# Optimization experiments

Hardware: AMD Instinct MI355X
Metric: run time of the kernel (lower is better)

The kernel has to match this reference:

```python
import jax, jax.numpy as jnp
import numpy as np

T, B = 128, 64
STATE_DIM, LATENT_DIM, AC_DIM, MS_DIM = 32, 16, 8, 8
STATE_EMBED, AC_EMBED, HIDDEN, OUT_DIM = 64, 16, 64, 18


def setup_inputs() -> dict:
    key = jax.random.key(0)
    ks = jax.random.split(key, 18)
    f = lambda i, shape: jax.random.normal(ks[i], shape, jnp.float32)
    s = 0.05  # param scale
    return dict(
        state=f(0, (T, B, STATE_DIM)),
        latent_mean=f(1, (T, B, LATENT_DIM)),
        latent_logvar=f(2, (T, B, LATENT_DIM)) * 0.1,
        latent_mean_t=f(3, (T, B, LATENT_DIM)),
        latent_logvar_t=f(4, (T, B, LATENT_DIM)) * 0.1,
        agent_character=f(5, (T, B, AC_DIM)),
        mental_state=f(6, (T, B, MS_DIM)),
        partner_actions=jax.random.randint(ks[7], (T, B), 0, OUT_DIM, jnp.int32),
        dones=(jax.random.uniform(ks[8], (T, B)) < 0.05).astype(jnp.float32),
        W_state=f(9, (STATE_DIM, STATE_EMBED)) * s, b_state=jnp.zeros(STATE_EMBED),
        W_ac=f(10, (AC_DIM, AC_EMBED)) * s, b_ac=jnp.zeros(AC_EMBED),
        W_embed=f(11, (STATE_EMBED + AC_EMBED, HIDDEN)) * s, b_embed=jnp.zeros(HIDDEN),
        W_hid=f(12, (AC_EMBED + MS_DIM, HIDDEN)) * s, b_hid=jnp.zeros(HIDDEN),
        Wi=f(13, (HIDDEN, 3 * HIDDEN)) * s, bi=jnp.zeros(3 * HIDDEN),
        Wh_rz=f(14, (HIDDEN, 2 * HIDDEN)) * s,
        Wh_n=f(15, (HIDDEN, HIDDEN)) * s, bh_n=jnp.zeros(HIDDEN),
        W_out=f(16, (HIDDEN, OUT_DIM)) * s, b_out=jnp.zeros(OUT_DIM),
    )


def reference(state, latent_mean, latent_logvar, latent_mean_t, latent_logvar_t,
              agent_character, mental_state, partner_actions, dones,
              W_state, b_state, W_ac, b_ac, W_embed, b_embed, W_hid, b_hid,
              Wi, bi, Wh_rz, Wh_n, bh_n, W_out, b_out):
    Tn = state.shape[0]
    # ---- KL between consecutive latent Gaussians (with N(0,I) prior at t=0) ----
    lm = jnp.concatenate((latent_mean, latent_mean_t), -1)      # (T,B,2L)
    lv = jnp.concatenate((latent_logvar, latent_logvar_t), -1)
    G = lm.shape[-1]
    am = jnp.concatenate((jnp.zeros((1,) + lm.shape[1:], lm.dtype), lm))
    al = jnp.concatenate((jnp.zeros((1,) + lv.shape[1:], lv.dtype), lv))
    mu, m = am[1:], am[:-1]
    logE, logS = al[1:], al[:-1]
    kl = 0.5 * (logS.sum(-1) - logE.sum(-1) - G
                + jnp.exp(logE - logS).sum(-1)
                + ((m - mu) ** 2 / jnp.exp(logS)).sum(-1))      # (T,B)
    kl_loss = kl.sum()
    # ---- feature extractors ----
    se = jax.nn.relu(state @ W_state + b_state)                 # (T,B,SE)
    ae = jax.nn.relu(agent_character @ W_ac + b_ac)             # (T,B,AE)
    embed = jnp.concatenate((se, ae), -1) @ W_embed + b_embed   # (T,B,H)
    hidden = jnp.concatenate((ae, mental_state), -1) @ W_hid + b_hid  # (T,B,H)
    # ---- k-batch: K=T shifted trajectories, zero-padded at the tail ----
    idx = jnp.arange(Tn)[:, None] + jnp.arange(Tn)[None, :]     # (K,T)
    valid = idx < Tn                                            # (K,T) bool
    cidx = jnp.minimum(idx, Tn - 1)
    vf = valid.astype(embed.dtype)[..., None]                   # (K,T,1)
    k_embed = embed[cidx] * vf[..., None]                       # (K,T,B,H)
    k_hidden = hidden[cidx] * vf[..., None]                     # (K,T,B,H)
    k_dones = dones[cidx] * vf                                  # (K,T,B)
    k_actions = jnp.where(valid[..., None], partner_actions[cidx], 0)  # (K,T,B)
    # fill_to_first_true: 1 up to and including the first done of each k-traj
    episode_mask = (jnp.cumsum(k_dones, axis=1) - k_dones == 0).astype(embed.dtype)  # (K,T,B)
    # ---- GRU scan over timestep axis, vectorized over (K,B) ----
    h0 = k_hidden[:, 0]                                         # (K,B,H)
    xs = (jnp.moveaxis(k_embed, 1, 0), jnp.moveaxis(k_hidden, 1, 0), jnp.moveaxis(k_dones, 1, 0))

    def step(h, x):
        x_t, h0_t, d_t = x                                      # (K,B,H),(K,B,H),(K,B)
        h = jnp.where(d_t[..., None] > 0, h0_t, h)              # reset on done
        ir, iz, i_n = jnp.split(x_t @ Wi + bi, 3, -1)
        hr, hz = jnp.split(h @ Wh_rz, 2, -1)
        r = jax.nn.sigmoid(ir + hr)
        z = jax.nn.sigmoid(iz + hz)
        n = jnp.tanh(i_n + r * (h @ Wh_n + bh_n))
        h_new = (1.0 - z) * n + z * h
        return h_new, h_new

    _, hs = jax.lax.scan(step, h0, xs)                          # (T,K,B,H)
    logp = jax.nn.log_softmax(hs @ W_out + b_out, -1)           # (T,K,B,O)
    k_act_t = jnp.moveaxis(k_actions, 1, 0)                     # (T,K,B)
    nll = -jnp.take_along_axis(logp, k_act_t[..., None], -1)[..., 0]  # (T,K,B)
    mask = valid.T[:, :, None].astype(nll.dtype) * jnp.moveaxis(episode_mask, 1, 0)
    recon_loss = (nll * mask).sum(axis=1)                       # sum over K -> (T,B)
    return kl_loss, recon_loss
```

## Files before the change

kernel.cpp:

```cpp
#include <hip/hip_runtime.h>


#define XI_OFF   0
#define HID_OFF  3145728
#define CTR_OFF  4194304

typedef float f32x16 __attribute__((ext_vector_type(16)));
typedef _Float16 h2 __attribute__((ext_vector_type(2)));

#if __has_builtin(__builtin_amdgcn_fdot2)
#define DOT2(a, b, c) __builtin_amdgcn_fdot2((a), (b), (c), false)
#else
#define DOT2(a, b, c) ((c) + (float)(a).x * (float)(b).x + (float)(a).y * (float)(b).y)
#endif

__device__ __forceinline__ h2 pack_pair(float h) {
  int hb = __builtin_bit_cast(int, h);
  int hp = __builtin_amdgcn_mov_dpp(hb, 0xB1, 0xF, 0xF, true);
  return __builtin_bit_cast(h2, __builtin_amdgcn_cvt_pkrtz(h, __builtin_bit_cast(float, hp)));
}

__global__ __launch_bounds__(256, 1) void precompute_kernel(
    const float* __restrict__ state, const float* __restrict__ ac, const float* __restrict__ ms,
    const float* __restrict__ Wst, const float* __restrict__ bst,
    const float* __restrict__ Wac, const float* __restrict__ bac,
    const float* __restrict__ Wem, const float* __restrict__ bem,
    const float* __restrict__ Whd, const float* __restrict__ bhd,
    const float* __restrict__ Wi,  const float* __restrict__ bi,
    const float* __restrict__ lm, const float* __restrict__ lv,
    const float* __restrict__ lmt, const float* __restrict__ lvt,
    _Float16* __restrict__ xi16, _Float16* __restrict__ hid16, float* __restrict__ out) {
  __shared__ float sWst[32 * 64];
  __shared__ float sWem[80 * 64];
  __shared__ float sWhd[24 * 64];
  __shared__ float sWac[8 * 16];
  __shared__ float sb[208];
  __shared__ float sin_[4][48];
  __shared__ float sse[4][80];
  __shared__ float semb[4][64];
  __shared__ float ps[4];
  int tid = threadIdx.x, lane = tid & 63, w = tid >> 6;

  if (blockIdx.x >= 256) {
    float total = 0.f;
    for (int it = 0; it < 16; ++it) {
      int idx = ((int)blockIdx.x - 256) * 256 + tid + it * 16384;
      int g = idx & 31;
      int pair = idx >> 5;
      const float* M = (g < 16) ? lm : lmt;
      const float* V = (g < 16) ? lv : lvt;
      int cur = pair * 16 + (g & 15);
      float mu = M[cur], lE = V[cur];
      float m = 0.f, lS = 0.f;
      if (pair >= 64) { m = M[cur - 1024]; lS = V[cur - 1024]; }
      float d = m - mu;
      total += 0.5f * (lS - lE - 1.f + __expf(lE - lS) + d * d * __expf(-lS));
    }
    #pragma unroll
    for (int off = 32; off; off >>= 1) total += __shfl_xor(total, off);
    if (lane == 0) ps[w] = total;
    __syncthreads();
    if (tid == 0) atomicAdd(out, ps[0] + ps[1] + ps[2] + ps[3]);
    return;
  }

  f32x16 wi0[4], wi1[4], wi2[4];
  #pragma unroll
  for (int k = 0; k < 64; ++k) {
    wi0[k >> 4][k & 15] = Wi[k * 192 + lane];
    wi1[k >> 4][k & 15] = Wi[k * 192 + 64 + lane];
    wi2[k >> 4][k & 15] = Wi[k * 192 + 128 + lane];
  }
  for (int i = tid; i < 32 * 64; i += 256) sWst[i] = Wst[i];
  for (int i = tid; i < 80 * 64; i += 256) sWem[i] = Wem[i];
  for (int i = tid; i < 24 * 64; i += 256) sWhd[i] = Whd[i];
  for (int i = tid; i < 8 * 16; i += 256) sWac[i] = Wac[i];
  if (tid < 64) sb[tid] = bst[tid];
  if (tid < 16) sb[64 + tid] = bac[tid];
  if (tid < 64) sb[80 + tid] = bem[tid];
  if (tid < 64) sb[144 + tid] = bhd[tid];
  float bi0 = bi[lane], bi1 = bi[64 + lane], bi2 = bi[128 + lane];
  __syncthreads();
  for (int cnt = 0; cnt < 8; ++cnt) {
    int pair = blockIdx.x * 32 + w * 8 + cnt;
    if (lane < 32)      sin_[w][lane] = state[pair * 32 + lane];
    else if (lane < 40) sin_[w][lane] = ac[pair * 8 + (lane - 32)];
    else if (lane < 48) sin_[w][lane] = ms[pair * 8 + (lane - 40)];
    __syncthreads();
    float se = sb[lane];
    #pragma unroll
    for (int k = 0; k < 32; ++k) se += sin_[w][k] * sWst[k * 64 + lane];
    se = fmaxf(se, 0.f);
    float ae = 0.f;
    if (lane < 16) {
      ae = sb[64 + lane];
      #pragma unroll
      for (int k = 0; k < 8; ++k) ae += sin_[w][32 + k] * sWac[k * 16 + lane];
      ae = fmaxf(ae, 0.f);
    }
    __syncthreads();
    sse[w][lane] = se;
    if (lane < 16) sse[w][64 + lane] = ae;
    __syncthreads();
    float em = sb[80 + lane];
    #pragma unroll
    for (int k = 0; k < 80; ++k) em += sse[w][k] * sWem[k * 64 + lane];
    float hd = sb[144 + lane];
    #pragma unroll
    for (int k = 0; k < 16; ++k) hd += sse[w][64 + k] * sWhd[k * 64 + lane];
    #pragma unroll
    for (int k = 0; k < 8; ++k) hd += sin_[w][40 + k] * sWhd[(16 + k) * 64 + lane];
    hid16[pair * 64 + lane] = (_Float16)hd;
    semb[w][lane] = em;
    __syncthreads();
    float x0 = bi0, x1 = bi1, x2 = bi2;
    #pragma unroll
    for (int k = 0; k < 64; ++k) {
      float e = semb[w][k];
      x0 += e * wi0[k >> 4][k & 15];
      x1 += e * wi1[k >> 4][k & 15];
      x2 += e * wi2[k >> 4][k & 15];
    }
    _Float16* xo = xi16 + pair * 192;
    xo[lane] = (_Float16)x0; xo[64 + lane] = (_Float16)x1; xo[128 + lane] = (_Float16)x2;
    __syncthreads();
  }
}

__global__ __launch_bounds__(64, 2) void rollout_kernel(
    const _Float16* __restrict__ xi16, const _Float16* __restrict__ hid16,
    const float* __restrict__ dones, const int* __restrict__ actions,
    const float* __restrict__ Whrz, const float* __restrict__ Whn,
    const float* __restrict__ bhn, const float* __restrict__ Wout,
    const float* __restrict__ bout, float* __restrict__ out,
    unsigned int* __restrict__ ctrs) {
  __shared__ __attribute__((aligned(16))) h2 sh2[32];
  __shared__ __attribute__((aligned(16))) float sloge[20];
  int lane = threadIdx.x;
  int row = (lane < 18) ? lane : 0;
  h2 Wr[32], Wz[32], Wn[32], Wo[32];
  #pragma unroll
  for (int k = 0; k < 32; ++k) {
    Wr[k] = h2{(_Float16)Whrz[(2 * k) * 128 + lane],      (_Float16)Whrz[(2 * k + 1) * 128 + lane]};
    Wz[k] = h2{(_Float16)Whrz[(2 * k) * 128 + 64 + lane], (_Float16)Whrz[(2 * k + 1) * 128 + 64 + lane]};
    Wn[k] = h2{(_Float16)Whn[(2 * k) * 64 + lane],        (_Float16)Whn[(2 * k + 1) * 64 + lane]};
    Wo[k] = h2{(_Float16)Wout[(2 * k) * 18 + row],        (_Float16)Wout[(2 * k + 1) * 18 + row]};
  }
  if (lane < 2) sloge[18 + lane] = 0.f;
  float bhn_r = bhn[lane];
  float bo_r = bout[row];
  __syncthreads();
  const uint4* shv = (const uint4*)sh2;
  int q = blockIdx.x & 7;
  while (true) {
    int i = 0;
    if (lane == 0) i = (int)atomicAdd(&ctrs[q], 1u);
    i = __shfl(i, 0);
    if (i >= 1024) break;
    int t = i >> 3, b = ((i & 7) << 3) | q;
    int u = t;
    int pr = (t << 6) | b;
    float h = (float)hid16[pr * 64 + lane];
    const _Float16* xb = xi16 + pr * 192;
    float x0 = (float)xb[lane], x1 = (float)xb[64 + lane], x2 = (float)xb[128 + lane];
    float d = dones[pr];
    int  act = actions[pr];
    if ((lane & 1) == 0) sh2[lane >> 1] = pack_pair(h);
    for (int s = 0;; ++s) {
      int un = (u < 127) ? u + 1 : 127;
      int prn = (un << 6) | b;
      const _Float16* xn = xi16 + prn * 192;
      float nx0 = (float)xn[lane], nx1 = (float)xn[64 + lane], nx2 = (float)xn[128 + lane];
      float nd = dones[prn];
      int   na = actions[prn];
      float nh = (float)hid16[prn * 64 + lane];
      float ara = x0, arb = 0.f, aza = x1, azb = 0.f, ana = 0.f, anb = 0.f;
      #pragma unroll
      for (int qq = 0; qq < 8; ++qq) {
        uint4 hv = shv[qq];
        h2 a0 = __builtin_bit_cast(h2, hv.x);
        h2 a1 = __builtin_bit_cast(h2, hv.y);
        h2 a2 = __builtin_bit_cast(h2, hv.z);
        h2 a3 = __builtin_bit_cast(h2, hv.w);
        ara = DOT2(a0, Wr[4 * qq + 0], ara); arb = DOT2(a1, Wr[4 * qq + 1], arb);
        ara = DOT2(a2, Wr[4 * qq + 2], ara); arb = DOT2(a3, Wr[4 * qq + 3], arb);
        aza = DOT2(a0, Wz[4 * qq + 0], aza); azb = DOT2(a1, Wz[4 * qq + 1], azb);
        aza = DOT2(a2, Wz[4 * qq + 2], aza); azb = DOT2(a3, Wz[4 * qq + 3], azb);
        ana = DOT2(a0, Wn[4 * qq + 0], ana); anb = DOT2(a1, Wn[4 * qq + 1], anb);
        ana = DOT2(a2, Wn[4 * qq + 2], ana); anb = DOT2(a3, Wn[4 * qq + 3], anb);
      }
      float ar = ara + arb, az = aza + azb, an = ana + anb;
      float r = __builtin_amdgcn_rcpf(1.f + __expf(-ar));
      float z = __builtin_amdgcn_rcpf(1.f + __expf(-az));
      float pre = x2 + r * (an + bhn_r);
      float n = 1.f - 2.f * __builtin_amdgcn_rcpf(1.f + __expf(2.f * pre));
      float hn = (1.f - z) * n + z * h;
      if ((lane & 1) == 0) sh2[lane >> 1] = pack_pair(hn);
      float la_a = bo_r, la_b = 0.f;
      #pragma unroll
      for (int qq = 0; qq < 8; ++qq) {
        uint4 hv = shv[qq];
        la_a = DOT2(__builtin_bit_cast(h2, hv.x), Wo[4 * qq + 0], la_a);
        la_b = DOT2(__builtin_bit_cast(h2, hv.y), Wo[4 * qq + 1], la_b);
        la_a = DOT2(__builtin_bit_cast(h2, hv.z), Wo[4 * qq + 2], la_a);
        la_b = DOT2(__builtin_bit_cast(h2, hv.w), Wo[4 * qq + 3], la_b);
      }
      float logit = la_a + la_b;
      if (lane < 18) sloge[lane] = __expf(logit);
      float4 e0 = *(const float4*)&sloge[0];
      float4 e1 = *(const float4*)&sloge[4];
      float4 e2 = *(const float4*)&sloge[8];
      float4 e3 = *(const float4*)&sloge[12];
      float4 e4 = *(const float4*)&sloge[16];
      float ssum = (((e0.x + e0.y) + (e0.z + e0.w)) + ((e1.x + e1.y) + (e1.z + e1.w)))
                 + (((e2.x + e2.y) + (e2.z + e2.w)) + ((e3.x + e3.y) + (e3.z + e3.w)))
                 + ((e4.x + e4.y) + (e4.z + e4.w));
      float la = __builtin_bit_cast(float, __builtin_amdgcn_readlane(__builtin_bit_cast(int, logit), act));
      float lse = __logf(ssum);
      if (lane == 0) atomicAdd(&out[1 + s * 64 + b], lse - la);
      if (d > 0.f || u == 127) break;
      u = un; x0 = nx0; x1 = nx1; x2 = nx2; d = nd; act = na;
      if (nd > 0.f) {
        h = nh;
        if ((lane & 1) == 0) sh2[lane >> 1] = pack_pair(h);
      } else {
        h = hn;
      }
    }
  }
}

extern "C" void kernel_launch(void* const* d_in, const int* in_sizes, int n_in,
                              void* d_out, int out_size, void* d_ws, size_t ws_size,
                              hipStream_t stream) {
  const float* state = (const float*)d_in[0];
  const float* lm    = (const float*)d_in[1];
  const float* lv    = (const float*)d_in[2];
  const float* lmt   = (const float*)d_in[3];
  const float* lvt   = (const float*)d_in[4];
  const float* ac    = (const float*)d_in[5];
  const float* ms    = (const float*)d_in[6];
  const int*   actions = (const int*)d_in[7];
  const float* dones = (const float*)d_in[8];
  const float* Wst = (const float*)d_in[9],  *bst = (const float*)d_in[10];
  const float* Wac = (const float*)d_in[11], *bac = (const float*)d_in[12];
  const float* Wem = (const float*)d_in[13], *bem = (const float*)d_in[14];
  const float* Whd = (const float*)d_in[15], *bhd = (const float*)d_in[16];
  const float* Wi  = (const float*)d_in[17], *bi  = (const float*)d_in[18];
  const float* Whrz = (const float*)d_in[19];
  const float* Whn  = (const float*)d_in[20], *bhn = (const float*)d_in[21];
  const float* Wout = (const float*)d_in[22], *bout = (const float*)d_in[23];
  float* out = (float*)d_out;
  _Float16* xi16  = (_Float16*)((char*)d_ws + XI_OFF);
  _Float16* hid16 = (_Float16*)((char*)d_ws + HID_OFF);
  unsigned int* ctrs = (unsigned int*)((char*)d_ws + CTR_OFF);

  hipMemsetAsync(d_out, 0, (size_t)out_size * sizeof(float), stream);
  hipMemsetAsync(ctrs, 0, 8 * sizeof(unsigned int), stream);

  hipLaunchKernelGGL(precompute_kernel, dim3(320), dim3(256), 0, stream,
                     state, ac, ms, Wst, bst, Wac, bac, Wem, bem, Whd, bhd, Wi, bi,
                     lm, lv, lmt, lvt, xi16, hid16, out);
  hipLaunchKernelGGL(rollout_kernel, dim3(2048), dim3(64), 0, stream,
                     xi16, hid16, dones, actions, Whrz, Whn, bhn, Wout, bout, out, ctrs);
}
```

Measured before the change: 177.5 us.

## Interleave xi and hidden rows, pack dones/actions, use DPP softmax sum

The precompute kernel now writes the input projections and hidden init into one 256-half row per (t,b). It also packs the done flag and action into a single int, so each rollout step issues fewer separate loads on its serial dependency chain. The softmax denominator is now summed with a DPP row scan plus two readlanes instead of LDS writes and float4 reads. The risk is extra DPP latency, and the hidden-state write is now interleaved into a larger row.

```diff
diff --git a/kernel.cpp b/kernel.cpp
--- a/kernel.cpp
+++ b/kernel.cpp
@@ -1,9 +1,9 @@
 #include <hip/hip_runtime.h>
 
 
-#define XI_OFF   0
-#define HID_OFF  3145728
-#define CTR_OFF  4194304
+#define XH_OFF   0
+#define AUX_OFF  4194304
+#define CTR_OFF  4227072
 
 typedef float f32x16 __attribute__((ext_vector_type(16)));
 typedef _Float16 h2 __attribute__((ext_vector_type(2)));
@@ -18,6 +18,19 @@
   int hb = __builtin_bit_cast(int, h);
   int hp = __builtin_amdgcn_mov_dpp(hb, 0xB1, 0xF, 0xF, true);
   return __builtin_bit_cast(h2, __builtin_amdgcn_cvt_pkrtz(h, __builtin_bit_cast(float, hp)));
+}
+
+__device__ __forceinline__ float row16_scan_add(float v) {
+  int t;
+  t = __builtin_amdgcn_update_dpp(0, __builtin_bit_cast(int, v), 0x111, 0xF, 0xF, true);
+  v += __builtin_bit_cast(float, t);
+  t = __builtin_amdgcn_update_dpp(0, __builtin_bit_cast(int, v), 0x112, 0xF, 0xF, true);
+  v += __builtin_bit_cast(float, t);
+  t = __builtin_amdgcn_update_dpp(0, __builtin_bit_cast(int, v), 0x114, 0xF, 0xF, true);
+  v += __builtin_bit_cast(float, t);
+  t = __builtin_amdgcn_update_dpp(0, __builtin_bit_cast(int, v), 0x118, 0xF, 0xF, true);
+  v += __builtin_bit_cast(float, t);
+  return v;
 }
 
 __global__ __launch_bounds__(256, 1) void precompute_kernel(
@@ -29,7 +42,8 @@
     const float* __restrict__ Wi,  const float* __restrict__ bi,
     const float* __restrict__ lm, const float* __restrict__ lv,
     const float* __restrict__ lmt, const float* __restrict__ lvt,
-    _Float16* __restrict__ xi16, _Float16* __restrict__ hid16, float* __restrict__ out) {
+    const float* __restrict__ dones, const int* __restrict__ actions,
+    _Float16* __restrict__ xh, int* __restrict__ aux, float* __restrict__ out) {
   __shared__ float sWst[32 * 64];
   __shared__ float sWem[80 * 64];
   __shared__ float sWhd[24 * 64];
@@ -86,6 +100,7 @@
     if (lane < 32)      sin_[w][lane] = state[pair * 32 + lane];
     else if (lane < 40) sin_[w][lane] = ac[pair * 8 + (lane - 32)];
     else if (lane < 48) sin_[w][lane] = ms[pair * 8 + (lane - 40)];
+    if (lane == 0) aux[pair] = (dones[pair] > 0.f ? (int)0x80000000 : 0) | actions[pair];
     __syncthreads();
     float se = sb[lane];
     #pragma unroll
@@ -110,7 +125,6 @@
     for (int k = 0; k < 16; ++k) hd += sse[w][64 + k] * sWhd[k * 64 + lane];
     #pragma unroll
     for (int k = 0; k < 8; ++k) hd += sin_[w][40 + k] * sWhd[(16 + k) * 64 + lane];
-    hid16[pair * 64 + lane] = (_Float16)hd;
     semb[w][lane] = em;
     __syncthreads();
     float x0 = bi0, x1 = bi1, x2 = bi2;
@@ -121,21 +135,20 @@
       x1 += e * wi1[k >> 4][k & 15];
       x2 += e * wi2[k >> 4][k & 15];
     }
-    _Float16* xo = xi16 + pair * 192;
-    xo[lane] = (_Float16)x0; xo[64 + lane] = (_Float16)x1; xo[128 + lane] = (_Float16)x2;
+    _Float16* xo = xh + pair * 256;
+    xo[lane] = (_Float16)x0; xo[64 + lane] = (_Float16)x1;
+    xo[128 + lane] = (_Float16)x2; xo[192 + lane] = (_Float16)hd;
     __syncthreads();
   }
 }
 
 __global__ __launch_bounds__(64, 2) void rollout_kernel(
-    const _Float16* __restrict__ xi16, const _Float16* __restrict__ hid16,
-    const float* __restrict__ dones, const int* __restrict__ actions,
+    const _Float16* __restrict__ xh, const int* __restrict__ aux,
     const float* __restrict__ Whrz, const float* __restrict__ Whn,
     const float* __restrict__ bhn, const float* __restrict__ Wout,
     const float* __restrict__ bout, float* __restrict__ out,
     unsigned int* __restrict__ ctrs) {
   __shared__ __attribute__((aligned(16))) h2 sh2[32];
-  __shared__ __attribute__((aligned(16))) float sloge[20];
   int lane = threadIdx.x;
   int row = (lane < 18) ? lane : 0;
   h2 Wr[32], Wz[32], Wn[32], Wo[32];
@@ -146,7 +159,6 @@
     Wn[k] = h2{(_Float16)Whn[(2 * k) * 64 + lane],        (_Float16)Whn[(2 * k + 1) * 64 + lane]};
     Wo[k] = h2{(_Float16)Wout[(2 * k) * 18 + row],        (_Float16)Wout[(2 * k + 1) * 18 + row]};
   }
-  if (lane < 2) sloge[18 + lane] = 0.f;
   float bhn_r = bhn[lane];
   float bo_r = bout[row];
   __syncthreads();
@@ -160,20 +172,18 @@
     int t = i >> 3, b = ((i & 7) << 3) | q;
     int u = t;
     int pr = (t << 6) | b;
-    float h = (float)hid16[pr * 64 + lane];
-    const _Float16* xb = xi16 + pr * 192;
+    const _Float16* xb = xh + pr * 256;
+    float h = (float)xb[192 + lane];
     float x0 = (float)xb[lane], x1 = (float)xb[64 + lane], x2 = (float)xb[128 + lane];
-    float d = dones[pr];
-    int  act = actions[pr];
+    int ax = aux[pr];
     if ((lane & 1) == 0) sh2[lane >> 1] = pack_pair(h);
     for (int s = 0;; ++s) {
       int un = (u < 127) ? u + 1 : 127;
       int prn = (un << 6) | b;
-      const _Float16* xn = xi16 + prn * 192;
+      const _Float16* xn = xh + prn * 256;
       float nx0 = (float)xn[lane], nx1 = (float)xn[64 + lane], nx2 = (float)xn[128 + lane];
-      float nd = dones[prn];
-      int   na = actions[prn];
-      float nh = (float)hid16[prn * 64 + lane];
+      float nh = (float)xn[192 + lane];
+      int nax = aux[prn];
       float ara = x0, arb = 0.f, aza = x1, azb = 0.f, ana = 0.f, anb = 0.f;
       #pragma unroll
       for (int qq = 0; qq < 8; ++qq) {
@@ -206,21 +216,17 @@
         la_b = DOT2(__builtin_bit_cast(h2, hv.w), Wo[4 * qq + 3], la_b);
       }
       float logit = la_a + la_b;
-      if (lane < 18) sloge[lane] = __expf(logit);
-      float4 e0 = *(const float4*)&sloge[0];
-      float4 e1 = *(const float4*)&sloge[4];
-      float4 e2 = *(const float4*)&sloge[8];
-      float4 e3 = *(const float4*)&sloge[12];
-      float4 e4 = *(const float4*)&sloge[16];
-      float ssum = (((e0.x + e0.y) + (e0.z + e0.w)) + ((e1.x + e1.y) + (e1.z + e1.w)))
-                 + (((e2.x + e2.y) + (e2.z + e2.w)) + ((e3.x + e3.y) + (e3.z + e3.w)))
-                 + ((e4.x + e4.y) + (e4.z + e4.w));
+      float e = (lane < 18) ? __expf(logit) : 0.f;
+      float er = row16_scan_add(e);
+      float ssum = __builtin_bit_cast(float, __builtin_amdgcn_readlane(__builtin_bit_cast(int, er), 15))
+                 + __builtin_bit_cast(float, __builtin_amdgcn_readlane(__builtin_bit_cast(int, er), 31));
+      int act = ax & 0xFFFF;
       float la = __builtin_bit_cast(float, __builtin_amdgcn_readlane(__builtin_bit_cast(int, logit), act));
       float lse = __logf(ssum);
       if (lane == 0) atomicAdd(&out[1 + s * 64 + b], lse - la);
-      if (d > 0.f || u == 127) break;
-      u = un; x0 = nx0; x1 = nx1; x2 = nx2; d = nd; act = na;
-      if (nd > 0.f) {
+      if (ax < 0 || u == 127) break;
+      u = un; x0 = nx0; x1 = nx1; x2 = nx2; ax = nax;
+      if (nax < 0) {
         h = nh;
         if ((lane & 1) == 0) sh2[lane >> 1] = pack_pair(h);
       } else {
@@ -251,8 +257,8 @@
   const float* Whn  = (const float*)d_in[20], *bhn = (const float*)d_in[21];
   const float* Wout = (const float*)d_in[22], *bout = (const float*)d_in[23];
   float* out = (float*)d_out;
-  _Float16* xi16  = (_Float16*)((char*)d_ws + XI_OFF);
-  _Float16* hid16 = (_Float16*)((char*)d_ws + HID_OFF);
+  _Float16* xh = (_Float16*)((char*)d_ws + XH_OFF);
+  int* aux = (int*)((char*)d_ws + AUX_OFF);
   unsigned int* ctrs = (unsigned int*)((char*)d_ws + CTR_OFF);
 
   hipMemsetAsync(d_out, 0, (size_t)out_size * sizeof(float), stream);
@@ -260,7 +266,7 @@
 
   hipLaunchKernelGGL(precompute_kernel, dim3(320), dim3(256), 0, stream,
                      state, ac, ms, Wst, bst, Wac, bac, Wem, bem, Whd, bhd, Wi, bi,
-                     lm, lv, lmt, lvt, xi16, hid16, out);
+                     lm, lv, lmt, lvt, dones, actions, xh, aux, out);
   hipLaunchKernelGGL(rollout_kernel, dim3(2048), dim3(64), 0, stream,
-                     xi16, hid16, dones, actions, Whrz, Whn, bhn, Wout, bout, out, ctrs);
-}
+                     xh, aux, Whrz, Whn, bhn, Wout, bout, out, ctrs);
+}
```

Result: slower. 186.1 us (+4.8%).
